# Optimization experiments

Measured on AMD Instinct MI355X. Metric: run time of the kernel, lower is better.

## Reference

```python
import jax, jax.numpy as jnp
import numpy as np

N = 50000      # nodes
E = 800000     # edges (before self-loops)
F_IN = 32      # num_node_features
H = 4          # heads
C = 64         # per-head channels (graph_hidden_channels // nheads)
HID = H * C    # 256
G = 1024       # number of graphs in batch
MLP_HID = 2048
NOUT = 768
NEG_SLOPE = 0.2


def setup_inputs() -> dict:
    key = jax.random.key(0)
    ks = jax.random.split(key, 24)
    def nrm(k, shape, s=0.05):
        return jax.random.normal(k, shape, jnp.float32) * s
    x = jax.random.normal(ks[0], (N, F_IN), jnp.float32)
    edge_index = jax.random.randint(ks[1], (2, E), 0, N)
    batch = jnp.sort(jax.random.randint(ks[2], (N,), 0, G))
    return {
        'x': x, 'edge_index': edge_index, 'batch': batch,
        'W1': nrm(ks[3], (F_IN, HID)), 'a_src1': nrm(ks[4], (H, C)), 'a_dst1': nrm(ks[5], (H, C)), 'b1': jnp.zeros((HID,), jnp.float32),
        'W2': nrm(ks[6], (HID, HID)), 'a_src2': nrm(ks[7], (H, C)), 'a_dst2': nrm(ks[8], (H, C)), 'b2': jnp.zeros((HID,), jnp.float32),
        'W3': nrm(ks[9], (HID, HID)), 'a_src3': nrm(ks[10], (H, C)), 'a_dst3': nrm(ks[11], (H, C)), 'b3': jnp.zeros((HID,), jnp.float32),
        'Wm1': nrm(ks[12], (HID, MLP_HID)), 'bm1': jnp.zeros((MLP_HID,), jnp.float32),
        'Wm2': nrm(ks[13], (MLP_HID, NOUT)), 'bm2': jnp.zeros((NOUT,), jnp.float32),
        'gamma': jnp.ones((NOUT,), jnp.float32), 'beta': jnp.zeros((NOUT,), jnp.float32),
    }


def _gat_layer(x, src, dst, W, a_s, a_d, b):
    # PyG GATConv (eval mode, dropout inactive), self-loops already in src/dst.
    h = (x @ W).reshape(N, H, C)                       # [N,H,C]
    ls = (h * a_s).sum(-1)                             # [N,H] source att logits
    ld = (h * a_d).sum(-1)                             # [N,H] target att logits
    logits = jax.nn.leaky_relu(ls[src] + ld[dst], NEG_SLOPE)  # [E',H]
    m = jax.ops.segment_max(logits, dst, num_segments=N)
    m = jnp.where(jnp.isfinite(m), m, 0.0)
    e = jnp.exp(logits - m[dst])
    denom = jax.ops.segment_sum(e, dst, num_segments=N) + 1e-16
    alpha = e / denom[dst]                             # segment softmax per dst node
    out = jax.ops.segment_sum(h[src] * alpha[:, :, None], dst, num_segments=N)
    return out.reshape(N, HID) + b


def reference(x, edge_index, batch, W1, a_src1, a_dst1, b1, W2, a_src2, a_dst2, b2,
              W3, a_src3, a_dst3, b3, Wm1, bm1, Wm2, bm2, gamma, beta):
    loop = jnp.arange(N)
    src = jnp.concatenate([edge_index[0], loop])
    dst = jnp.concatenate([edge_index[1], loop])
    h = jax.nn.relu(_gat_layer(x, src, dst, W1, a_src1, a_dst1, b1))
    h = jax.nn.relu(_gat_layer(h, src, dst, W2, a_src2, a_dst2, b2))
    h = _gat_layer(h, src, dst, W3, a_src3, a_dst3, b3)
    # global_mean_pool
    sums = jax.ops.segment_sum(h, batch, num_segments=G)
    counts = jax.ops.segment_sum(jnp.ones((N, 1), jnp.float32), batch, num_segments=G)
    pooled = sums / jnp.maximum(counts, 1.0)           # [G,HID]
    z = jax.nn.relu(pooled @ Wm1 + bm1)
    z = z @ Wm2 + bm2
    mu = z.mean(-1, keepdims=True)
    var = z.var(-1, keepdims=True)
    return gamma * (z - mu) * jax.lax.rsqrt(var + 1e-5) + beta
```

## Files before the change

kernel.cpp:

```cpp
#include <hip/hip_runtime.h>
#include <math.h>

#define N_NODES 50000
#define N_EDGES 800000
#define N_ETOT  850000
#define F_IN    32
#define HEADS   4
#define CHAN    64
#define HID     256
#define NGRAPH  1024
#define MLP_HID 2048
#define NOUT    768
#define NEG_SLOPE 0.2f
#define KSPL    4

typedef __attribute__((ext_vector_type(8))) short short8v;
typedef __attribute__((ext_vector_type(4))) float f32x4;

__device__ __forceinline__ unsigned short f2bf(float f) {
    unsigned u = __float_as_uint(f);
    u += 0x7fff + ((u >> 16) & 1);
    return (unsigned short)(u >> 16);
}
__device__ __forceinline__ float bf2f(unsigned short s) {
    return __uint_as_float((unsigned)s << 16);
}

__global__ __launch_bounds__(256) void hist_kernel(const int* __restrict__ ei,
                                                   int* __restrict__ deg) {
    int e = blockIdx.x * 256 + threadIdx.x;
    if (e >= N_ETOT) return;
    int d = (e < N_EDGES) ? ei[N_EDGES + e] : (e - N_EDGES);
    atomicAdd(&deg[d], 1);
}

__global__ __launch_bounds__(1024) void scan_kernel(const int* __restrict__ deg,
                                                    int* __restrict__ off,
                                                    int* __restrict__ cur) {
    __shared__ int sums[1024];
    const int t = threadIdx.x;
    const int CHK = (N_NODES + 1023) / 1024;
    int lo = t * CHK;
    int hi = min(lo + CHK, N_NODES);
    int s = 0;
    for (int i = lo; i < hi; ++i) s += deg[i];
    sums[t] = s;
    __syncthreads();
    for (int d = 1; d < 1024; d <<= 1) {
        int v = (t >= d) ? sums[t - d] : 0;
        __syncthreads();
        sums[t] += v;
        __syncthreads();
    }
    int run = sums[t] - s;
    for (int i = lo; i < hi; ++i) {
        int d0 = deg[i];
        off[i] = run;
        cur[i] = run;
        run += d0;
    }
    if (t == 1023) off[N_NODES] = run;
}

__global__ __launch_bounds__(256) void scatter_kernel(const int* __restrict__ ei,
                                                      int* __restrict__ cur,
                                                      int* __restrict__ ssrc) {
    int e = blockIdx.x * 256 + threadIdx.x;
    if (e >= N_ETOT) return;
    int s, d;
    if (e < N_EDGES) { s = ei[e]; d = ei[N_EDGES + e]; }
    else             { s = e - N_EDGES; d = s; }
    int pos = atomicAdd(&cur[d], 1);
    ssrc[pos] = s;
}

__global__ __launch_bounds__(256) void castT_kernel(const float* __restrict__ W,
                                                    unsigned short* __restrict__ Wt) {
    const int r = blockIdx.x;
    const int c = threadIdx.x;
    Wt[(size_t)c * HID + r] = f2bf(W[(size_t)r * HID + c]);
}

__global__ __launch_bounds__(256) void gemm_mfma_bt(const float* __restrict__ A,
                                                    const unsigned short* __restrict__ Bt,
                                                    float* __restrict__ C,
                                                    int M) {
    __shared__ unsigned short Asb[64][32];
    __shared__ unsigned short Bsb[64][32];
    const int t = threadIdx.x;
    const int wave = t >> 6;
    const int lane = t & 63;
    const int bm = blockIdx.x * 64;
    const int bn = blockIdx.y * 64;
    const int sr = t >> 2;
    const int skq = (t & 3) * 8;
    const int fr = lane & 15;
    const int fq = lane >> 4;

    f32x4 acc[4] = {{0.f,0.f,0.f,0.f},{0.f,0.f,0.f,0.f},
                    {0.f,0.f,0.f,0.f},{0.f,0.f,0.f,0.f}};

    for (int k0 = 0; k0 < HID; k0 += 32) {
        {
            const int gr = bm + sr;
            float4 v0 = make_float4(0.f,0.f,0.f,0.f), v1 = v0;
            if (gr < M) {
                v0 = *(const float4*)&A[(size_t)gr * HID + k0 + skq];
                v1 = *(const float4*)&A[(size_t)gr * HID + k0 + skq + 4];
            }
            ushort4 q0, q1;
            q0.x = f2bf(v0.x); q0.y = f2bf(v0.y); q0.z = f2bf(v0.z); q0.w = f2bf(v0.w);
            q1.x = f2bf(v1.x); q1.y = f2bf(v1.y); q1.z = f2bf(v1.z); q1.w = f2bf(v1.w);
            *(ushort4*)&Asb[sr][skq]     = q0;
            *(ushort4*)&Asb[sr][skq + 4] = q1;
        }
        *(short8v*)&Bsb[sr][skq] =
            *(const short8v*)&Bt[(size_t)(bn + sr) * HID + k0 + skq];
        __syncthreads();

        short8v a = *(short8v*)&Asb[wave * 16 + fr][fq * 8];
        #pragma unroll
        for (int nt = 0; nt < 4; ++nt) {
            short8v b = *(short8v*)&Bsb[nt * 16 + fr][fq * 8];
            acc[nt] = __builtin_amdgcn_mfma_f32_16x16x32_bf16(a, b, acc[nt], 0, 0, 0);
        }
        __syncthreads();
    }

    #pragma unroll
    for (int nt = 0; nt < 4; ++nt) {
        #pragma unroll
        for (int r = 0; r < 4; ++r) {
            int row = bm + wave * 16 + fq * 4 + r;
            if (row < M)
                C[(size_t)row * HID + bn + nt * 16 + fr] = acc[nt][r];
        }
    }
}

template <int BM, int BN, int TM, int TN, bool BIAS, bool RELU, bool SPLITK>
__global__ __launch_bounds__(256) void gemm_kernel(const float* __restrict__ A,
                                                   const float* __restrict__ B,
                                                   const float* __restrict__ bias,
                                                   float* __restrict__ C,
                                                   int M, int Nn, int K, int lda) {
    __shared__ float As[16][BM + 4];
    __shared__ float Bs[16][BN + 4];
    if (SPLITK) {
        const int z = blockIdx.z;
        A += (size_t)z * K;
        B += (size_t)z * K * Nn;
        C += (size_t)z * M * Nn;
    }
    const int t = threadIdx.x;
    const int bm = blockIdx.x * BM;
    const int bn = blockIdx.y * BN;
    constexpr int NTX = BN / TN;
    const int tx = t % NTX;
    const int ty = t / NTX;
    const int row0 = ty * TM;
    const int col0 = tx * TN;
    constexpr int BN4 = BN / 4;
    constexpr int AITER = BM * 4 / 256;
    constexpr int BITER = 16 * BN4 / 256;

    float acc[TM][TN] = {};
    for (int k0 = 0; k0 < K; k0 += 16) {
        #pragma unroll
        for (int it = 0; it < AITER; ++it) {
            int f = t + it * 256;
            int m = f >> 2, kq = (f & 3) << 2;
            int gr = bm + m;
            float4 v = make_float4(0.f, 0.f, 0.f, 0.f);
            if (gr < M) v = *(const float4*)&A[(size_t)gr * lda + k0 + kq];
            As[kq + 0][m] = v.x;
            As[kq + 1][m] = v.y;
            As[kq + 2][m] = v.z;
            As[kq + 3][m] = v.w;
        }
        #pragma unroll
        for (int it = 0; it < BITER; ++it) {
            int f = t + it * 256;
            int k = f / BN4, n = (f % BN4) << 2;
            *(float4*)&Bs[k][n] = *(const float4*)&B[(size_t)(k0 + k) * Nn + bn + n];
        }
        __syncthreads();
        #pragma unroll
        for (int k = 0; k < 16; ++k) {
            float a[TM], b[TN];
            #pragma unroll
            for (int i = 0; i < TM; i += 4)
                *(float4*)&a[i] = *(const float4*)&As[k][row0 + i];
            #pragma unroll
            for (int j = 0; j < TN; j += 4)
                *(float4*)&b[j] = *(const float4*)&Bs[k][col0 + j];
            #pragma unroll
            for (int i = 0; i < TM; ++i)
                #pragma unroll
                for (int j = 0; j < TN; ++j)
                    acc[i][j] += a[i] * b[j];
        }
        __syncthreads();
    }
    #pragma unroll
    for (int i = 0; i < TM; ++i) {
        int r = bm + row0 + i;
        if (r >= M) continue;
        #pragma unroll
        for (int j = 0; j < TN; j += 4) {
            int c = bn + col0 + j;
            float4 v;
            v.x = acc[i][j + 0];
            v.y = acc[i][j + 1];
            v.z = acc[i][j + 2];
            v.w = acc[i][j + 3];
            if (BIAS) {
                const float4 bv = *(const float4*)&bias[c];
                v.x += bv.x; v.y += bv.y; v.z += bv.z; v.w += bv.w;
            }
            if (RELU) {
                v.x = fmaxf(v.x, 0.f); v.y = fmaxf(v.y, 0.f);
                v.z = fmaxf(v.z, 0.f); v.w = fmaxf(v.w, 0.f);
            }
            *(float4*)&C[(size_t)r * Nn + c] = v;
        }
    }
}

__global__ __launch_bounds__(256) void logits_kernel(const float* __restrict__ h,
                                                     const float* __restrict__ a_s,
                                                     const float* __restrict__ a_d,
                                                     float* __restrict__ ls,
                                                     float* __restrict__ ld,
                                                     unsigned short* __restrict__ hb) {
    const int lane = threadIdx.x & 63;
    const int wid  = threadIdx.x >> 6;
    const int node = blockIdx.x * 4 + wid;
    if (node >= N_NODES) return;
    const int myh = lane >> 4;

    float4 v = *(const float4*)&h[(size_t)node * HID + lane * 4];
    ushort4 q;
    q.x = f2bf(v.x); q.y = f2bf(v.y); q.z = f2bf(v.z); q.w = f2bf(v.w);
    *(ushort4*)&hb[(size_t)node * HID + lane * 4] = q;

    const float4 as4 = *(const float4*)&a_s[lane * 4];
    const float4 ad4 = *(const float4*)&a_d[lane * 4];
    float ss = v.x * as4.x + v.y * as4.y + v.z * as4.z + v.w * as4.w;
    float dd = v.x * ad4.x + v.y * ad4.y + v.z * ad4.z + v.w * ad4.w;
    #pragma unroll
    for (int o = 1; o < 16; o <<= 1) {
        ss += __shfl_xor(ss, o);
        dd += __shfl_xor(dd, o);
    }
    if ((lane & 15) == 0) {
        ls[node * HEADS + myh] = ss;
        ld[node * HEADS + myh] = dd;
    }
}

__device__ __forceinline__ float leaky(float x) { return fmaxf(x, NEG_SLOPE * x); }

template <bool RELU>
__global__ __launch_bounds__(256) void gat_aggregate(const unsigned short* __restrict__ hb,
                                                     const int* __restrict__ off,
                                                     const int* __restrict__ ssrc,
                                                     const float* __restrict__ ls,
                                                     const float* __restrict__ ld,
                                                     const float* __restrict__ bias,
                                                     float* __restrict__ h_out) {
    const int lane = threadIdx.x & 63;
    const int wid  = threadIdx.x >> 6;
    const int node = blockIdx.x * 4 + wid;
    if (node >= N_NODES) return;
    const int lo = off[node], hi = off[node + 1];
    const int myh = lane >> 4;
    const float ldv = ld[node * HEADS + myh];

    float4 acc = make_float4(0.f, 0.f, 0.f, 0.f);
    float den = 0.f;
    int e = lo;
    for (; e + 2 <= hi; e += 2) {
        int s0 = ssrc[e];
        int s1 = ssrc[e + 1];
        float l0 = ls[s0 * HEADS + myh];
        float l1 = ls[s1 * HEADS + myh];
        ushort4 q0 = *(const ushort4*)&hb[(size_t)s0 * HID + lane * 4];
        ushort4 q1 = *(const ushort4*)&hb[(size_t)s1 * HID + lane * 4];
        float w0 = __expf(leaky(l0 + ldv));
        float w1 = __expf(leaky(l1 + ldv));
        den += w0 + w1;
        acc.x += w0 * bf2f(q0.x) + w1 * bf2f(q1.x);
        acc.y += w0 * bf2f(q0.y) + w1 * bf2f(q1.y);
        acc.z += w0 * bf2f(q0.z) + w1 * bf2f(q1.z);
        acc.w += w0 * bf2f(q0.w) + w1 * bf2f(q1.w);
    }
    if (e < hi) {
        int s0 = ssrc[e];
        float w0 = __expf(leaky(ls[s0 * HEADS + myh] + ldv));
        ushort4 q0 = *(const ushort4*)&hb[(size_t)s0 * HID + lane * 4];
        den += w0;
        acc.x += w0 * bf2f(q0.x); acc.y += w0 * bf2f(q0.y);
        acc.z += w0 * bf2f(q0.z); acc.w += w0 * bf2f(q0.w);
    }
    float inv = 1.f / (den + 1e-16f);
    float4 bv = *(const float4*)(bias + lane * 4);
    float4 o;
    o.x = acc.x * inv + bv.x; o.y = acc.y * inv + bv.y;
    o.z = acc.z * inv + bv.z; o.w = acc.w * inv + bv.w;
    if (RELU) {
        o.x = fmaxf(o.x, 0.f); o.y = fmaxf(o.y, 0.f);
        o.z = fmaxf(o.z, 0.f); o.w = fmaxf(o.w, 0.f);
    }
    *(float4*)(h_out + (size_t)node * HID + lane * 4) = o;
}

__global__ __launch_bounds__(256) void pool_kernel(const float* __restrict__ h,
                                                   const int* __restrict__ batch,
                                                   float* __restrict__ pooled) {
    const int g = blockIdx.x;
    __shared__ int bounds[2];
    if (threadIdx.x < 2) {
        int target = g + threadIdx.x;
        int lo = 0, hi = N_NODES;
        while (lo < hi) {
            int mid = (lo + hi) >> 1;
            if (batch[mid] < target) lo = mid + 1; else hi = mid;
        }
        bounds[threadIdx.x] = lo;
    }
    __syncthreads();
    const int lo = bounds[0], hi = bounds[1];
    const int c = threadIdx.x;
    float s = 0.f;
    for (int i = lo; i < hi; ++i) s += h[(size_t)i * HID + c];
    float cnt = (float)max(hi - lo, 1);
    pooled[(size_t)g * HID + c] = s / cnt;
}

__global__ __launch_bounds__(256) void ln_kernel(const float* __restrict__ z2p,
                                                 const float* __restrict__ bm2,
                                                 const float* __restrict__ gamma,
                                                 const float* __restrict__ beta,
                                                 float* __restrict__ out) {
    const int row = blockIdx.x;
    float v[3];
    float s = 0.f, s2 = 0.f;
    #pragma unroll
    for (int i = 0; i < 3; ++i) {
        int c = threadIdx.x + i * 256;
        float a = bm2[c];
        #pragma unroll
        for (int sp = 0; sp < KSPL; ++sp)
            a += z2p[(size_t)sp * NGRAPH * NOUT + (size_t)row * NOUT + c];
        v[i] = a;
        s += a;
        s2 += a * a;
    }
    #pragma unroll
    for (int o = 32; o > 0; o >>= 1) {
        s  += __shfl_down(s, o);
        s2 += __shfl_down(s2, o);
    }
    __shared__ float red[8];
    const int wid = threadIdx.x >> 6, lane = threadIdx.x & 63;
    if (lane == 0) { red[wid] = s; red[4 + wid] = s2; }
    __syncthreads();
    if (threadIdx.x == 0) {
        float S  = red[0] + red[1] + red[2] + red[3];
        float S2 = red[4] + red[5] + red[6] + red[7];
        float mu  = S / NOUT;
        float var = S2 / NOUT - mu * mu;
        red[0] = mu;
        red[1] = rsqrtf(var + 1e-5f);
    }
    __syncthreads();
    float mu = red[0], rstd = red[1];
    #pragma unroll
    for (int i = 0; i < 3; ++i) {
        int c = threadIdx.x + i * 256;
        out[(size_t)row * NOUT + c] = gamma[c] * (v[i] - mu) * rstd + beta[c];
    }
}

extern "C" void kernel_launch(void* const* d_in, const int* in_sizes, int n_in,
                              void* d_out, int out_size, void* d_ws, size_t ws_size,
                              hipStream_t stream) {
    const float* x     = (const float*)d_in[0];
    const int*   ei    = (const int*)d_in[1];
    const int*   batch = (const int*)d_in[2];
    const float* W1    = (const float*)d_in[3];
    const float* a_s1  = (const float*)d_in[4];
    const float* a_d1  = (const float*)d_in[5];
    const float* b1    = (const float*)d_in[6];
    const float* W2    = (const float*)d_in[7];
    const float* a_s2  = (const float*)d_in[8];
    const float* a_d2  = (const float*)d_in[9];
    const float* b2    = (const float*)d_in[10];
    const float* W3    = (const float*)d_in[11];
    const float* a_s3  = (const float*)d_in[12];
    const float* a_d3  = (const float*)d_in[13];
    const float* b3    = (const float*)d_in[14];
    const float* Wm1   = (const float*)d_in[15];
    const float* bm1   = (const float*)d_in[16];
    const float* Wm2   = (const float*)d_in[17];
    const float* bm2   = (const float*)d_in[18];
    const float* gamma = (const float*)d_in[19];
    const float* beta  = (const float*)d_in[20];
    float* out = (float*)d_out;

    char* p = (char*)d_ws;
    auto alloc = [&](size_t bytes) {
        void* r = (void*)p;
        p += (bytes + 255) & ~(size_t)255;
        return r;
    };
    int*   deg    = (int*)  alloc((size_t)N_NODES * 4);
    int*   off    = (int*)  alloc((size_t)(N_NODES + 1) * 4);
    int*   cur    = (int*)  alloc((size_t)N_NODES * 4);
    int*   ssrc   = (int*)  alloc((size_t)N_ETOT * 4);
    float* ls     = (float*)alloc((size_t)N_NODES * HEADS * 4);
    float* ld     = (float*)alloc((size_t)N_NODES * HEADS * 4);
    float* hA     = (float*)alloc((size_t)N_NODES * HID * 4);
    float* hB     = (float*)alloc((size_t)N_NODES * HID * 4);
    unsigned short* hb  = (unsigned short*)alloc((size_t)N_NODES * HID * 2);
    unsigned short* W2t = (unsigned short*)alloc((size_t)HID * HID * 2);
    unsigned short* W3t = (unsigned short*)alloc((size_t)HID * HID * 2);
    float* pooled = (float*)alloc((size_t)NGRAPH * HID * 4);
    float* z1     = (float*)alloc((size_t)NGRAPH * MLP_HID * 4);
    float* z2p    = (float*)alloc((size_t)KSPL * NGRAPH * NOUT * 4);

    hipMemsetAsync(deg, 0, (size_t)N_NODES * 4, stream);
    hist_kernel<<<(N_ETOT + 255) / 256, 256, 0, stream>>>(ei, deg);
    scan_kernel<<<1, 1024, 0, stream>>>(deg, off, cur);
    scatter_kernel<<<(N_ETOT + 255) / 256, 256, 0, stream>>>(ei, cur, ssrc);
    castT_kernel<<<HID, 256, 0, stream>>>(W2, W2t);
    castT_kernel<<<HID, 256, 0, stream>>>(W3, W3t);

    const int nodeBlocks = (N_NODES + 3) / 4;
    dim3 mfmaGrid((N_NODES + 63) / 64, HID / 64);

    dim3 gemmN((N_NODES + 127) / 128, HID / 128);
    gemm_kernel<128, 128, 8, 8, false, false, false><<<gemmN, 256, 0, stream>>>(x, W1, nullptr, hA, N_NODES, HID, F_IN, F_IN);
    logits_kernel<<<nodeBlocks, 256, 0, stream>>>(hA, a_s1, a_d1, ls, ld, hb);
    gat_aggregate<true><<<nodeBlocks, 256, 0, stream>>>(hb, off, ssrc, ls, ld, b1, hB);

    gemm_mfma_bt<<<mfmaGrid, 256, 0, stream>>>(hB, W2t, hA, N_NODES);
    logits_kernel<<<nodeBlocks, 256, 0, stream>>>(hA, a_s2, a_d2, ls, ld, hb);
    gat_aggregate<true><<<nodeBlocks, 256, 0, stream>>>(hb, off, ssrc, ls, ld, b2, hB);

    gemm_mfma_bt<<<mfmaGrid, 256, 0, stream>>>(hB, W3t, hA, N_NODES);
    logits_kernel<<<nodeBlocks, 256, 0, stream>>>(hA, a_s3, a_d3, ls, ld, hb);
    gat_aggregate<false><<<nodeBlocks, 256, 0, stream>>>(hb, off, ssrc, ls, ld, b3, hB);

    pool_kernel<<<NGRAPH, 256, 0, stream>>>(hB, batch, pooled);
    dim3 gm1(NGRAPH / 64, MLP_HID / 128);
    gemm_kernel<64, 128, 4, 8, true, true, false><<<gm1, 256, 0, stream>>>(pooled, Wm1, bm1, z1, NGRAPH, MLP_HID, HID, HID);
    dim3 gm2(NGRAPH / 64, NOUT / 64, KSPL);
    gemm_kernel<64, 64, 4, 4, false, false, true><<<gm2, 256, 0, stream>>>(z1, Wm2, nullptr, z2p, NGRAPH, NOUT, MLP_HID / KSPL, MLP_HID);
    ln_kernel<<<NGRAPH, 256, 0, stream>>>(z2p, bm2, gamma, beta, out);
}
```

Baseline: 763.6 us.

## Replace single-block degree scan with multi-block three-phase prefix scan

Result: faster. 659.3 us (-13.7%).

```diff
diff --git a/kernel.cpp b/kernel.cpp
--- a/kernel.cpp
+++ b/kernel.cpp
@@ -13,6 +13,7 @@
 #define NOUT    768
 #define NEG_SLOPE 0.2f
 #define KSPL    4
+#define NBLK    ((N_NODES + 255) / 256)
 
 typedef __attribute__((ext_vector_type(8))) short short8v;
 typedef __attribute__((ext_vector_type(4))) float f32x4;
@@ -34,32 +35,58 @@
     atomicAdd(&deg[d], 1);
 }
 
-__global__ __launch_bounds__(1024) void scan_kernel(const int* __restrict__ deg,
+__global__ __launch_bounds__(256) void bsum_kernel(const int* __restrict__ deg,
+                                                   int* __restrict__ bsum) {
+    const int t = threadIdx.x;
+    int i = blockIdx.x * 256 + t;
+    int v = (i < N_NODES) ? deg[i] : 0;
+    #pragma unroll
+    for (int o = 32; o > 0; o >>= 1) v += __shfl_down(v, o);
+    __shared__ int red[4];
+    if ((t & 63) == 0) red[t >> 6] = v;
+    __syncthreads();
+    if (t == 0) bsum[blockIdx.x] = red[0] + red[1] + red[2] + red[3];
+}
+
+__global__ __launch_bounds__(256) void bscan_kernel(const int* __restrict__ bsum,
+                                                    int* __restrict__ bpre,
+                                                    int* __restrict__ off) {
+    __shared__ int s[256];
+    const int t = threadIdx.x;
+    int v = (t < NBLK) ? bsum[t] : 0;
+    s[t] = v;
+    __syncthreads();
+    for (int d = 1; d < 256; d <<= 1) {
+        int u = (t >= d) ? s[t - d] : 0;
+        __syncthreads();
+        s[t] += u;
+        __syncthreads();
+    }
+    if (t < NBLK) bpre[t] = s[t] - v;
+    if (t == NBLK - 1) off[N_NODES] = s[t];
+}
+
+__global__ __launch_bounds__(256) void cscan_kernel(const int* __restrict__ deg,
+                                                    const int* __restrict__ bpre,
                                                     int* __restrict__ off,
                                                     int* __restrict__ cur) {
-    __shared__ int sums[1024];
+    __shared__ int s[256];
     const int t = threadIdx.x;
-    const int CHK = (N_NODES + 1023) / 1024;
-    int lo = t * CHK;
-    int hi = min(lo + CHK, N_NODES);
-    int s = 0;
-    for (int i = lo; i < hi; ++i) s += deg[i];
-    sums[t] = s;
-    __syncthreads();
-    for (int d = 1; d < 1024; d <<= 1) {
-        int v = (t >= d) ? sums[t - d] : 0;
-        __syncthreads();
-        sums[t] += v;
-        __syncthreads();
-    }
-    int run = sums[t] - s;
-    for (int i = lo; i < hi; ++i) {
-        int d0 = deg[i];
-        off[i] = run;
-        cur[i] = run;
-        run += d0;
-    }
-    if (t == 1023) off[N_NODES] = run;
+    const int i = blockIdx.x * 256 + t;
+    int v = (i < N_NODES) ? deg[i] : 0;
+    s[t] = v;
+    __syncthreads();
+    for (int d = 1; d < 256; d <<= 1) {
+        int u = (t >= d) ? s[t - d] : 0;
+        __syncthreads();
+        s[t] += u;
+        __syncthreads();
+    }
+    if (i < N_NODES) {
+        int pre = bpre[blockIdx.x] + s[t] - v;
+        off[i] = pre;
+        cur[i] = pre;
+    }
 }
 
 __global__ __launch_bounds__(256) void scatter_kernel(const int* __restrict__ ei,
@@ -419,6 +446,8 @@
     int*   off    = (int*)  alloc((size_t)(N_NODES + 1) * 4);
     int*   cur    = (int*)  alloc((size_t)N_NODES * 4);
     int*   ssrc   = (int*)  alloc((size_t)N_ETOT * 4);
+    int*   bsum   = (int*)  alloc((size_t)256 * 4);
+    int*   bpre   = (int*)  alloc((size_t)256 * 4);
     float* ls     = (float*)alloc((size_t)N_NODES * HEADS * 4);
     float* ld     = (float*)alloc((size_t)N_NODES * HEADS * 4);
     float* hA     = (float*)alloc((size_t)N_NODES * HID * 4);
@@ -432,7 +461,9 @@
 
     hipMemsetAsync(deg, 0, (size_t)N_NODES * 4, stream);
     hist_kernel<<<(N_ETOT + 255) / 256, 256, 0, stream>>>(ei, deg);
-    scan_kernel<<<1, 1024, 0, stream>>>(deg, off, cur);
+    bsum_kernel<<<NBLK, 256, 0, stream>>>(deg, bsum);
+    bscan_kernel<<<1, 256, 0, stream>>>(bsum, bpre, off);
+    cscan_kernel<<<NBLK, 256, 0, stream>>>(deg, bpre, off, cur);
     scatter_kernel<<<(N_ETOT + 255) / 256, 256, 0, stream>>>(ei, cur, ssrc);
     castT_kernel<<<HID, 256, 0, stream>>>(W2, W2t);
     castT_kernel<<<HID, 256, 0, stream>>>(W3, W3t);
```
